# Kernel tuning notes

Measured on AMD Instinct MI355X. Metric: run time of the kernel, lower is better.

## Reference

```python
import jax, jax.numpy as jnp
import numpy as np

CHANS = [32, 32, 64, 64, 128, 128]
IN_CHANS = [1, 32, 32, 64, 64, 128]
BETA = 0.25  # VectorQuantizer_reset default; ResidualVQ's beta=0.4 is never forwarded
BN_EPS = 1e-5


def setup_inputs() -> dict:
    key = jax.random.key(0)
    ks = jax.random.split(key, 20)
    B, L, IDIM, H, NE = 64, 2000, 80, 256, 1024
    inp = {"speech": jax.random.normal(ks[0], (B, L, IDIM), jnp.float32)}
    for i, (ci, co) in enumerate(zip(IN_CHANS, CHANS)):
        inp[f"cw{i}"] = jax.random.normal(ks[1 + i], (co, ci, 3, 3), jnp.float32) * 0.05
        inp[f"g{i}"] = jnp.ones((co,), jnp.float32)
        inp[f"b{i}"] = jnp.zeros((co,), jnp.float32)
    inp["w_ih"] = jax.random.normal(ks[10], (3 * H, 256), jnp.float32) * 0.05
    inp["w_hh"] = jax.random.normal(ks[11], (3 * H, H), jnp.float32) * 0.05
    inp["bih"] = jnp.zeros((3 * H,), jnp.float32)
    inp["bhh"] = jnp.zeros((3 * H,), jnp.float32)
    for j, k in zip((1, 2, 3), (12, 13, 14)):
        inp[f"cb{j}"] = jax.random.uniform(ks[k], (NE, H), jnp.float32, -1.0 / NE, 1.0 / NE)
    return inp


def conv_bn_relu(x, w, g, b):
    # Conv2d(k=3, stride=2, pad=1, bias=False) + BatchNorm2d (training-mode batch stats) + ReLU
    y = jax.lax.conv_general_dilated(x, w, (2, 2), [(1, 1), (1, 1)],
                                     dimension_numbers=("NCHW", "OIHW", "NCHW"))
    mu = jnp.mean(y, axis=(0, 2, 3), keepdims=True)
    var = jnp.mean((y - mu) ** 2, axis=(0, 2, 3), keepdims=True)  # biased, as torch BN
    y = (y - mu) * jax.lax.rsqrt(var + BN_EPS) * g.reshape(1, -1, 1, 1) + b.reshape(1, -1, 1, 1)
    return jax.nn.relu(y)


def gru_last_hidden(x, w_ih, w_hh, bih, bhh):
    # x: (B, T, D). PyTorch GRU, 1 layer, h0 = 0; returns last hidden state (B, H).
    B = x.shape[0]
    H = w_hh.shape[1]
    xw = jnp.einsum("btd,gd->btg", x, w_ih) + bih  # (B, T, 3H), precompute input gates

    def step(h, xt):
        gh = h @ w_hh.T + bhh
        i_r, i_z, i_n = jnp.split(xt, 3, axis=-1)
        h_r, h_z, h_n = jnp.split(gh, 3, axis=-1)
        r = jax.nn.sigmoid(i_r + h_r)
        z = jax.nn.sigmoid(i_z + h_z)
        n = jnp.tanh(i_n + r * h_n)
        return (1.0 - z) * n + z * h, None

    h0 = jnp.zeros((B, H), x.dtype)
    hT, _ = jax.lax.scan(step, h0, jnp.swapaxes(xw, 0, 1))
    return hT


def vq(z, E):
    # z: (B, e_dim), E: (n_e, e_dim). Nearest-neighbor quantize + straight-through.
    d = jnp.sum(z * z, axis=1, keepdims=True) + jnp.sum(E * E, axis=1) - 2.0 * (z @ E.T)
    idx = jnp.argmin(d, axis=1)  # (B,)
    z_q = E[idx]
    loss = jnp.mean((jax.lax.stop_gradient(z_q) - z) ** 2) \
         + BETA * jnp.mean((z_q - jax.lax.stop_gradient(z)) ** 2)
    z_q_st = z + jax.lax.stop_gradient(z_q - z)
    return z_q_st, loss, idx


def reference(speech, cw0, g0, b0, cw1, g1, b1, cw2, g2, b2, cw3, g3, b3,
              cw4, g4, b4, cw5, g5, b5, w_ih, w_hh, bih, bhh, cb1, cb2, cb3):
    x = speech[:, None, :, :]  # (B, 1, L, idim)
    for w, g, b in ((cw0, g0, b0), (cw1, g1, b1), (cw2, g2, b2),
                    (cw3, g3, b3), (cw4, g4, b4), (cw5, g5, b5)):
        x = conv_bn_relu(x, w, g, b)
    B, C, T, F = x.shape
    hs = x.transpose(0, 2, 1, 3).reshape(B, T, C * F)  # (B, T', C*F)
    ref_embs = gru_last_hidden(hs, w_ih, w_hh, bih, bhh)  # (B, 256)

    residual = ref_embs
    zq1, l1, i1 = vq(residual, cb1)
    residual = residual - zq1
    zq2, l2, i2 = vq(residual, cb2)
    residual = residual - zq2
    zq3, l3, i3 = vq(residual, cb3)

    z_q_out = jnp.concatenate([zq1, zq2, zq3], axis=1)  # (B, 3*e_dim)
    vq_loss = l1 + l2 + l3
    codebooks = (zq1, zq2, zq3, zq1 + zq2 + zq3)
    return (z_q_out, vq_loss, i1[:, None], codebooks)
```

## Files before the change

### kernel.cpp

```cpp
#include <hip/hip_runtime.h>
#include <math.h>


__global__ void transpose_kernel(const float* __restrict__ in, float* __restrict__ out,
                                 int R, int C) {
  int n = R * C;
  for (int t = blockIdx.x * blockDim.x + threadIdx.x; t < n; t += gridDim.x * blockDim.x) {
    int i = t / C, j = t % C;
    out[j * R + i] = in[t];
  }
}

__global__ __launch_bounds__(256) void se_kernel(const float* __restrict__ ET,
                                                 float* __restrict__ sE) {
  int c = blockIdx.x * 256 + threadIdx.x;
  float s = 0.f;
  for (int k = 0; k < 256; ++k) {
    float v = ET[k * 1024 + c];
    s = fmaf(v, v, s);
  }
  sE[c] = s;
}

__global__ __launch_bounds__(256) void conv0_stats_kernel(
    const float* __restrict__ speech, const float* __restrict__ w0,
    float* __restrict__ part) {
  constexpr int TS = 81, TH = 49, TN = TH * TS;
  __shared__ float sp[TN];
  const int tid = threadIdx.x;
  const int bx = blockIdx.x;
  const int b = blockIdx.z;
  const int to0 = bx * 24;
  const int sr0 = 2 * to0 - 1;
  const float* sb = speech + (size_t)b * 2000 * 80;
  for (int i = tid; i < TN; i += 256) {
    int r = i / TS, c = i % TS;
    int gr = sr0 + r, gc = c - 1;
    sp[i] = (gr >= 0 && gr < 2000 && gc >= 0 && gc < 80) ? sb[gr * 80 + gc] : 0.f;
  }
  __syncthreads();

  const int fo = tid % 40;
  const int trr = tid / 40;
  const bool rowok = (trr < 6);
  const int r0 = rowok ? trr * 4 : 0;

  float xv4[4][9];
  {
    int sb0 = (2 * r0) * TS + 2 * fo;
    float p0 = sp[sb0], p1 = sp[sb0 + 1], p2 = sp[sb0 + 2];
#pragma unroll
    for (int k = 0; k < 4; ++k) {
      int mr = (2 * (r0 + k) + 1) * TS + 2 * fo;
      xv4[k][0] = p0; xv4[k][1] = p1; xv4[k][2] = p2;
      xv4[k][3] = sp[mr]; xv4[k][4] = sp[mr + 1]; xv4[k][5] = sp[mr + 2];
      xv4[k][6] = sp[mr + TS]; xv4[k][7] = sp[mr + TS + 1]; xv4[k][8] = sp[mr + TS + 2];
      p0 = xv4[k][6]; p1 = xv4[k][7]; p2 = xv4[k][8];
    }
  }
  bool val[4];
#pragma unroll
  for (int k = 0; k < 4; ++k) val[k] = rowok && (to0 + r0 + k < 1000);

  float s[32], q[32];
#pragma unroll
  for (int c = 0; c < 32; ++c) { s[c] = 0.f; q[c] = 0.f; }
#pragma unroll
  for (int c = 0; c < 32; ++c) {
    const float* wk = w0 + c * 9;
    float w0v = wk[0], w1v = wk[1], w2v = wk[2], w3v = wk[3], w4v = wk[4];
    float w5v = wk[5], w6v = wk[6], w7v = wk[7], w8v = wk[8];
#pragma unroll
    for (int k = 0; k < 4; ++k) {
      float a = xv4[k][0] * w0v;
      a = fmaf(xv4[k][1], w1v, a); a = fmaf(xv4[k][2], w2v, a);
      a = fmaf(xv4[k][3], w3v, a); a = fmaf(xv4[k][4], w4v, a);
      a = fmaf(xv4[k][5], w5v, a); a = fmaf(xv4[k][6], w6v, a);
      a = fmaf(xv4[k][7], w7v, a); a = fmaf(xv4[k][8], w8v, a);
      if (val[k]) { s[c] += a; q[c] = fmaf(a, a, q[c]); }
    }
  }
  const int wid = tid >> 6;
  const int lane = tid & 63;
  const int pidx = ((b * 42 + bx) << 2) | wid;
#pragma unroll
  for (int c = 0; c < 32; ++c) {
    float ss = s[c], qq = q[c];
#pragma unroll
    for (int m = 32; m >= 1; m >>= 1) {
      ss += __shfl_xor(ss, m, 64);
      qq += __shfl_xor(qq, m, 64);
    }
    if (lane == 0) {
      part[(size_t)c * 10752 + pidx] = ss;
      part[(size_t)(32 + c) * 10752 + pidx] = qq;
    }
  }
}

__global__ __launch_bounds__(256) void conv1_fused_kernel(
    const float* __restrict__ speech, const float* __restrict__ w0,
    const float* __restrict__ aff0, const float* __restrict__ w1,
    float* __restrict__ y) {
  constexpr int SPS = 81, SPH = 51, SPN = SPH * SPS;
  constexpr int LTS = 43, LTH = 25;
  __shared__ float sp[SPN];
  __shared__ float l0t[2][LTH * LTS];
  const int tid = threadIdx.x;
  const int bx = blockIdx.x;
  const int b = blockIdx.z;
  const int to0 = bx * 12;
  const int l0r0 = 2 * to0 - 1;
  const int sr0 = 4 * to0 - 3;
  const float* sb = speech + (size_t)b * 2000 * 80;
  for (int i = tid; i < SPN; i += 256) {
    int r = i / SPS, c = i % SPS;
    int gr = sr0 + r, gc = c - 1;
    sp[i] = (gr >= 0 && gr < 2000 && gc >= 0 && gc < 80) ? sb[gr * 80 + gc] : 0.f;
  }

  const int fc = tid % 42;
  const int fr0 = tid / 42;
  const bool filler = (tid < 210);
  const int wcol = fc - 1;
  const bool colok = (wcol >= 0) && (wcol < 40);
  const int spc = colok ? (2 * wcol) : 0;
  const int r0 = fr0 * 5;

  const int fo = tid % 20;
  const int tr = tid / 20;
  const int to = to0 + tr;
  const bool active = (tr < 12) && (to < 500);
  const int trc = (tr < 12) ? tr : 0;

  float acc[32];
#pragma unroll
  for (int c = 0; c < 32; ++c) acc[c] = 0.f;

  __syncthreads();

#define L0FILL(CIDX, BF)                                                      \
  if (filler) {                                                               \
    const float* wk = w0 + (CIDX) * 9;                                        \
    const float wv0 = wk[0], wv1 = wk[1], wv2 = wk[2], wv3 = wk[3];           \
    const float wv4 = wk[4], wv5 = wk[5], wv6 = wk[6], wv7 = wk[7];           \
    const float wv8 = wk[8];                                                  \
    const float sc = aff0[CIDX], sh = aff0[32 + (CIDX)];                      \
    int sb0 = (2 * r0) * SPS + spc;                                           \
    float t0 = sp[sb0], t1 = sp[sb0 + 1], t2 = sp[sb0 + 2];                   \
    _Pragma("unroll")                                                         \
    for (int k = 0; k < 5; ++k) {                                             \
      int r = r0 + k;                                                         \
      int mr = (2 * r + 1) * SPS + spc;                                       \
      float m0 = sp[mr], m1 = sp[mr + 1], m2 = sp[mr + 2];                    \
      float b0 = sp[mr + SPS], b1 = sp[mr + SPS + 1], b2 = sp[mr + SPS + 2];  \
      float a = t0 * wv0;                                                     \
      a = fmaf(t1, wv1, a); a = fmaf(t2, wv2, a);                             \
      a = fmaf(m0, wv3, a); a = fmaf(m1, wv4, a); a = fmaf(m2, wv5, a);       \
      a = fmaf(b0, wv6, a); a = fmaf(b1, wv7, a); a = fmaf(b2, wv8, a);       \
      int h0 = l0r0 + r;                                                      \
      bool ok = colok && h0 >= 0 && h0 < 1000;                                \
      float vv = ok ? fmaxf(fmaf(a, sc, sh), 0.f) : 0.f;                      \
      l0t[BF][r * LTS + fc] = vv;                                             \
      t0 = b0; t1 = b1; t2 = b2;                                              \
    }                                                                         \
  }

  L0FILL(0, 0)
  __syncthreads();

  for (int ci = 0; ci < 32; ++ci) {
    int cur = ci & 1;
    if (ci + 1 < 32) { L0FILL(ci + 1, cur ^ 1) }
    float xv[9];
    int base = 2 * trc * LTS + 2 * fo;
#pragma unroll
    for (int t = 0; t < 9; ++t) xv[t] = l0t[cur][base + (t / 3) * LTS + (t % 3)];
    const float* wp = w1 + ci * 9;
#pragma unroll
    for (int c = 0; c < 32; ++c) {
      const float* wc = wp + (size_t)c * 32 * 9;
#pragma unroll
      for (int t = 0; t < 9; ++t) acc[c] = fmaf(xv[t], wc[t], acc[c]);
    }
    __syncthreads();
  }
#undef L0FILL

  if (active) {
#pragma unroll
    for (int c = 0; c < 32; ++c)
      y[(((size_t)b * 32 + c) * 500 + to) * 20 + fo] = acc[c];
  }
}

template <int CI, int COG, int WO, int ROWS, int WI, int HI, int HO>
__global__ __launch_bounds__(256) void conv_kernel(
    const float* __restrict__ x, const float* __restrict__ w,
    const float* __restrict__ aff, float* __restrict__ y, int CO) {
  constexpr int TW = WI + 2;
  constexpr int TS = (TW & 1) ? TW : TW + 1;
  constexpr int TH = 2 * ROWS + 1;
  constexpr int TN = TH * TW;
  constexpr int F = (TN + 255) / 256;
  __shared__ float tile[2][TH * TS];

  const int tid = threadIdx.x;
  const int fo = tid % WO;
  const int tr = tid / WO;
  const int to0 = blockIdx.x * ROWS;
  const int to = to0 + tr;
  const int co0 = blockIdx.y * COG;
  const int b = blockIdx.z;
  const bool active = (tr < ROWS) && (to < HO);
  const int trc = (tr < ROWS) ? tr : 0;

  int fa[F], fof[F];
  bool fv[F], fw[F];
#pragma unroll
  for (int j = 0; j < F; ++j) {
    int i = tid + j * 256;
    int r = i / TW, c = i % TW;
    int gih = 2 * to0 - 1 + r;
    int giw = c - 1;
    bool inb = (i < TN);
    bool v = inb && gih >= 0 && gih < HI && giw >= 0 && giw < WI;
    fw[j] = inb;
    fv[j] = v;
    fof[j] = v ? (gih * WI + giw) : 0;
    fa[j] = inb ? (r * TS + c) : 0;
  }

  float acc[COG];
#pragma unroll
  for (int c = 0; c < COG; ++c) acc[c] = 0.f;

  const float* xb = x + (size_t)b * CI * HI * WI;

  {
    const float sc = aff[0], sh = aff[CI];
#pragma unroll
    for (int j = 0; j < F; ++j) {
      if (fw[j]) {
        float v = xb[fof[j]];
        v = fv[j] ? fmaxf(fmaf(v, sc, sh), 0.f) : 0.f;
        tile[0][fa[j]] = v;
      }
    }
  }
  __syncthreads();

  for (int ci = 0; ci < CI; ++ci) {
    int cur = ci & 1;
    if (ci + 1 < CI) {
      const float* xc = xb + (size_t)(ci + 1) * HI * WI;
      const float sc = aff[ci + 1], sh = aff[CI + ci + 1];
#pragma unroll
      for (int j = 0; j < F; ++j) {
        if (fw[j]) {
          float v = xc[fof[j]];
          v = fv[j] ? fmaxf(fmaf(v, sc, sh), 0.f) : 0.f;
          tile[cur ^ 1][fa[j]] = v;
        }
      }
    }
    float xv[9];
    int base = 2 * trc * TS + 2 * fo;
#pragma unroll
    for (int t = 0; t < 9; ++t) xv[t] = tile[cur][base + (t / 3) * TS + (t % 3)];
    const float* wp = w + ((size_t)co0 * CI + ci) * 9;
#pragma unroll
    for (int c = 0; c < COG; ++c) {
      const float* wc = wp + (size_t)c * CI * 9;
#pragma unroll
      for (int t = 0; t < 9; ++t) acc[c] = fmaf(xv[t], wc[t], acc[c]);
    }
    __syncthreads();
  }

  if (active) {
#pragma unroll
    for (int c = 0; c < COG; ++c)
      y[(((size_t)b * CO + co0 + c) * HO + to) * WO + fo] = acc[c];
  }
}

__global__ __launch_bounds__(256) void conv5_kernel(
    const float* __restrict__ x, const float* __restrict__ w5,
    const float* __restrict__ aff, float* __restrict__ part5) {
  constexpr int TS = 5, TH = 65, TN = TH * TS;
  __shared__ float tile[2][TN];
  const int tid = threadIdx.x;
  const int p = tid & 63;
  const int to = p >> 1, fo = p & 1;
  const int cog = tid >> 6;
  const int co0 = cog * 32;
  const int ci0 = blockIdx.y * 32;
  const int b = blockIdx.z;

  int fa[2], fof[2];
  bool fv[2], fw[2];
#pragma unroll
  for (int j = 0; j < 2; ++j) {
    int i = tid + j * 256;
    int r = i / TS, c = i % TS;
    int gih = r - 1, giw = c - 1;
    bool inb = (i < TN);
    bool v = inb && gih >= 0 && gih < 63 && giw >= 0 && giw < 3;
    fw[j] = inb; fv[j] = v;
    fof[j] = v ? (gih * 3 + giw) : 0;
    fa[j] = inb ? i : 0;
  }

  float acc[32];
#pragma unroll
  for (int c = 0; c < 32; ++c) acc[c] = 0.f;

  const float* xb = x + (size_t)b * 128 * 189;

  {
    const float sc = aff[ci0], sh = aff[128 + ci0];
    const float* xc = xb + (size_t)ci0 * 189;
#pragma unroll
    for (int j = 0; j < 2; ++j) {
      if (fw[j]) {
        float v = xc[fof[j]];
        v = fv[j] ? fmaxf(fmaf(v, sc, sh), 0.f) : 0.f;
        tile[0][fa[j]] = v;
      }
    }
  }
  __syncthreads();

  for (int cc = 0; cc < 32; ++cc) {
    int cur = cc & 1;
    int ci = ci0 + cc;
    if (cc + 1 < 32) {
      const float* xc = xb + (size_t)(ci + 1) * 189;
      const float sc = aff[ci + 1], sh = aff[128 + ci + 1];
#pragma unroll
      for (int j = 0; j < 2; ++j) {
        if (fw[j]) {
          float v = xc[fof[j]];
          v = fv[j] ? fmaxf(fmaf(v, sc, sh), 0.f) : 0.f;
          tile[cur ^ 1][fa[j]] = v;
        }
      }
    }
    float xv[9];
#pragma unroll
    for (int t = 0; t < 9; ++t)
      xv[t] = tile[cur][(2 * to + t / 3) * TS + 2 * fo + (t % 3)];
    const float* wp = w5 + ((size_t)co0 * 128 + ci) * 9;
#pragma unroll
    for (int c = 0; c < 32; ++c) {
      const float* wc = wp + (size_t)c * 128 * 9;
#pragma unroll
      for (int t = 0; t < 9; ++t) acc[c] = fmaf(xv[t], wc[t], acc[c]);
    }
    __syncthreads();
  }

#pragma unroll
  for (int c = 0; c < 32; ++c)
    part5[(((size_t)blockIdx.y * 64 + b) * 128 + co0 + c) * 64 + p] = acc[c];
}

__global__ __launch_bounds__(256) void reduce4_kernel(const float* __restrict__ p,
                                                      float* __restrict__ y) {
  int i = blockIdx.x * 256 + threadIdx.x;
  if (i < 524288)
    y[i] = p[i] + p[i + 524288] + p[i + 2 * 524288] + p[i + 3 * 524288];
}

__global__ __launch_bounds__(256) void stats_kernel(const float* __restrict__ x,
                                                    float* __restrict__ part,
                                                    int C, int HW) {
  int c = blockIdx.x, b = blockIdx.y, tid = threadIdx.x;
  const float* xb = x + ((size_t)b * C + c) * HW;
  float s = 0.f, q = 0.f;
  for (int i = tid; i < HW; i += 256) {
    float v = xb[i];
    s += v;
    q = fmaf(v, v, q);
  }
#pragma unroll
  for (int m = 32; m >= 1; m >>= 1) {
    s += __shfl_xor(s, m, 64);
    q += __shfl_xor(q, m, 64);
  }
  if ((tid & 63) == 0) {
    int w = tid >> 6;
    part[(size_t)c * 256 + b * 4 + w] = s;
    part[(size_t)(C + c) * 256 + b * 4 + w] = q;
  }
}

__global__ __launch_bounds__(256) void bn_finalize(
    const float* __restrict__ part, const float* __restrict__ g,
    const float* __restrict__ bb, float* __restrict__ aff, int CO, int P,
    double invN) {
  __shared__ double s1[256];
  __shared__ double s2[256];
  int c = blockIdx.x, tid = threadIdx.x;
  double a = 0, q = 0;
  for (int i = tid; i < P; i += 256) {
    a += (double)part[(size_t)c * P + i];
    q += (double)part[(size_t)(CO + c) * P + i];
  }
  s1[tid] = a;
  s2[tid] = q;
  __syncthreads();
  for (int s = 128; s > 0; s >>= 1) {
    if (tid < s) { s1[tid] += s1[tid + s]; s2[tid] += s2[tid + s]; }
    __syncthreads();
  }
  if (tid == 0) {
    double mean = s1[0] * invN;
    double var = s2[0] * invN - mean * mean;
    float scale = g[c] * (float)(1.0 / sqrt(var + 1e-5));
    aff[c] = scale;
    aff[CO + c] = bb[c] - (float)mean * scale;
  }
}

__global__ __launch_bounds__(256) void hs_kernel(const float* __restrict__ raw,
                                                 const float* __restrict__ aff5,
                                                 float* __restrict__ hs) {
  int i = blockIdx.x * 256 + threadIdx.x;
  if (i >= 524288) return;
  int b = i >> 13;
  int j = i & 8191;
  int t = j >> 8;
  int d = j & 255;
  int c = d >> 1;
  int f = d & 1;
  float sc = aff5[c], sh = aff5[128 + c];
  float v = raw[(((size_t)b * 128 + c) * 32 + t) * 2 + f];
  hs[i] = fmaxf(fmaf(v, sc, sh), 0.f);
}

__global__ __launch_bounds__(256) void xw_kernel(const float* __restrict__ hs,
                                                 const float* __restrict__ w_ihT,
                                                 const float* __restrict__ bih,
                                                 float* __restrict__ xw) {
  __shared__ float sh[8 * 256];
  int tid = threadIdx.x;
  int bt0 = blockIdx.x * 8;
  for (int i = tid; i < 8 * 256; i += 256) sh[i] = hs[(size_t)bt0 * 256 + i];
  __syncthreads();
  float acc[3][8];
#pragma unroll
  for (int g = 0; g < 3; ++g)
#pragma unroll
    for (int r = 0; r < 8; ++r) acc[g][r] = 0.f;
  for (int k = 0; k < 256; ++k) {
    float w0 = w_ihT[k * 768 + tid];
    float w1 = w_ihT[k * 768 + 256 + tid];
    float w2 = w_ihT[k * 768 + 512 + tid];
#pragma unroll
    for (int r = 0; r < 8; ++r) {
      float hv = sh[r * 256 + k];
      acc[0][r] = fmaf(hv, w0, acc[0][r]);
      acc[1][r] = fmaf(hv, w1, acc[1][r]);
      acc[2][r] = fmaf(hv, w2, acc[2][r]);
    }
  }
  float b0 = bih[tid], b1 = bih[256 + tid], b2 = bih[512 + tid];
  for (int r = 0; r < 8; ++r) {
    size_t base = (size_t)(bt0 + r) * 768;
    xw[base + tid] = acc[0][r] + b0;
    xw[base + 256 + tid] = acc[1][r] + b1;
    xw[base + 512 + tid] = acc[2][r] + b2;
  }
}

__global__ __launch_bounds__(768) void gru_kernel(const float* __restrict__ xw,
                                                  const float* __restrict__ w_hhT,
                                                  const float* __restrict__ bhh,
                                                  float* __restrict__ zout) {
  __shared__ __align__(16) float h[256];
  __shared__ float gh[768];
  int b = blockIdx.x, j = threadIdx.x;
  if (j < 256) h[j] = 0.f;
  __syncthreads();
  float bh = bhh[j];
  for (int t = 0; t < 32; ++t) {
    float acc = 0.f;
    const float4* h4 = (const float4*)h;
#pragma unroll 8
    for (int k4 = 0; k4 < 64; ++k4) {
      float4 hv = h4[k4];
      const float* wr = w_hhT + (4 * k4) * 768 + j;
      acc = fmaf(hv.x, wr[0], acc);
      acc = fmaf(hv.y, wr[768], acc);
      acc = fmaf(hv.z, wr[1536], acc);
      acc = fmaf(hv.w, wr[2304], acc);
    }
    gh[j] = acc + bh;
    __syncthreads();
    float hnew = 0.f;
    if (j < 256) {
      const float* xt = xw + ((size_t)b * 32 + t) * 768;
      float ir = xt[j], iz = xt[256 + j], inn = xt[512 + j];
      float r = 1.f / (1.f + expf(-(ir + gh[j])));
      float zz = 1.f / (1.f + expf(-(iz + gh[256 + j])));
      float n = tanhf(fmaf(r, gh[512 + j], inn));
      hnew = (1.f - zz) * n + zz * h[j];
    }
    __syncthreads();
    if (j < 256) h[j] = hnew;
    __syncthreads();
  }
  if (j < 256) zout[(size_t)b * 256 + j] = h[j];
}

template <int FIRST, int LAST>
__global__ __launch_bounds__(256) void vq_stage(
    const float* __restrict__ rin, const float* __restrict__ ET,
    const float* __restrict__ sE, const float* __restrict__ E,
    float* __restrict__ zq1, float* __restrict__ zq2, float* __restrict__ rout,
    float* __restrict__ msep, float* __restrict__ i1out,
    const float* __restrict__ z0, float* __restrict__ zqsum) {
  __shared__ float rz[256];
  __shared__ float rs[256];
  __shared__ int ri[256];
  __shared__ int bidx;
  int b = blockIdx.x, tid = threadIdx.x;
  rz[tid] = rin[(size_t)b * 256 + tid];
  __syncthreads();
  float a0 = 0.f, a1 = 0.f, a2 = 0.f, a3 = 0.f;
  for (int k = 0; k < 256; ++k) {
    float zk = rz[k];
    const float* row = ET + (size_t)k * 1024 + tid;
    a0 = fmaf(zk, row[0], a0);
    a1 = fmaf(zk, row[256], a1);
    a2 = fmaf(zk, row[512], a2);
    a3 = fmaf(zk, row[768], a3);
  }
  float s0 = sE[tid] - 2.f * a0;
  float s1 = sE[256 + tid] - 2.f * a1;
  float s2 = sE[512 + tid] - 2.f * a2;
  float s3 = sE[768 + tid] - 2.f * a3;
  float bs = s0;
  int bi = tid;
  if (s1 < bs) { bs = s1; bi = 256 + tid; }
  if (s2 < bs) { bs = s2; bi = 512 + tid; }
  if (s3 < bs) { bs = s3; bi = 768 + tid; }
  rs[tid] = bs;
  ri[tid] = bi;
  __syncthreads();
  for (int s = 128; s > 0; s >>= 1) {
    if (tid < s) {
      float os = rs[tid + s];
      int oi = ri[tid + s];
      if (os < rs[tid] || (os == rs[tid] && oi < ri[tid])) { rs[tid] = os; ri[tid] = oi; }
    }
    __syncthreads();
  }
  if (tid == 0) {
    bidx = ri[0];
    if (FIRST) i1out[b] = (float)ri[0];
  }
  __syncthreads();
  int idx = bidx;
  float zq = E[(size_t)idx * 256 + tid];
  float rv = rz[tid];
  float d = zq - rv;
  float rn = rv - zq;
  zq1[(size_t)b * 768 + tid] = zq;
  zq2[(size_t)b * 256 + tid] = zq;
  rout[(size_t)b * 256 + tid] = rn;
  if (LAST) zqsum[(size_t)b * 256 + tid] = z0[(size_t)b * 256 + tid] - rn;
  rs[tid] = d * d;
  __syncthreads();
  for (int s = 128; s > 0; s >>= 1) {
    if (tid < s) rs[tid] += rs[tid + s];
    __syncthreads();
  }
  if (tid == 0) msep[b] = rs[0];
}

__global__ void loss_kernel(const float* __restrict__ msep, float* __restrict__ out) {
  if (threadIdx.x == 0 && blockIdx.x == 0) {
    float s = 0.f;
    for (int i = 0; i < 192; ++i) s += msep[i];
    out[0] = 1.25f * s / 16384.0f;
  }
}

extern "C" void kernel_launch(void* const* d_in, const int* in_sizes, int n_in,
                              void* d_out, int out_size, void* d_ws, size_t ws_size,
                              hipStream_t stream) {
  const float* speech = (const float*)d_in[0];
  const float* cw[6];
  const float* gg[6];
  const float* bbp[6];
  for (int i = 0; i < 6; ++i) {
    cw[i] = (const float*)d_in[1 + 3 * i];
    gg[i] = (const float*)d_in[2 + 3 * i];
    bbp[i] = (const float*)d_in[3 + 3 * i];
  }
  const float* w_ih = (const float*)d_in[19];
  const float* w_hh = (const float*)d_in[20];
  const float* bih = (const float*)d_in[21];
  const float* bhh = (const float*)d_in[22];
  const float* cb[3] = {(const float*)d_in[23], (const float*)d_in[24], (const float*)d_in[25]};
  float* out = (float*)d_out;
  float* ws_f = (float*)d_ws;
  (void)in_sizes; (void)n_in; (void)out_size;

  size_t off = 0;
  float* act1 = ws_f + off; off += 20480000ull;
  float* act2 = ws_f + off; off += 10240000ull;
  float* act3 = ws_f + off; off += 2560000ull;
  float* part = ws_f + off; off += 700000ull;
  float* affs = ws_f + off; off += 1536ull;
  float* w_ihT = ws_f + off; off += 196608ull;
  float* w_hhT = ws_f + off; off += 196608ull;
  float* hs = ws_f + off; off += 524288ull;
  float* xw = ws_f + off; off += 1572864ull;
  float* zb = ws_f + off; off += 16384ull;
  float* rA = ws_f + off; off += 16384ull;
  float* rB = ws_f + off; off += 16384ull;
  float* ET0 = ws_f + off; off += 262144ull;
  float* ET1 = ws_f + off; off += 262144ull;
  float* ET2 = ws_f + off; off += 262144ull;
  float* sEp = ws_f + off; off += 3072ull;
  float* msep = ws_f + off; off += 192ull;

  if (ws_size < off * sizeof(float)) return;

  float* part5 = act1;
  float* act4 = act2;
  float* act5 = act3;

  const size_t OFF_LOSS = 49152;
  const size_t OFF_I1 = 49153;
  const size_t OFF_CB1 = 49217;
  const size_t OFF_CB2 = 65601;
  const size_t OFF_CB3 = 81985;
  const size_t OFF_CBSUM = 98369;

  transpose_kernel<<<256, 256, 0, stream>>>(w_ih, w_ihT, 768, 256);
  transpose_kernel<<<256, 256, 0, stream>>>(w_hh, w_hhT, 768, 256);
  transpose_kernel<<<256, 256, 0, stream>>>(cb[0], ET0, 1024, 256);
  transpose_kernel<<<256, 256, 0, stream>>>(cb[1], ET1, 1024, 256);
  transpose_kernel<<<256, 256, 0, stream>>>(cb[2], ET2, 1024, 256);
  se_kernel<<<4, 256, 0, stream>>>(ET0, sEp);
  se_kernel<<<4, 256, 0, stream>>>(ET1, sEp + 1024);
  se_kernel<<<4, 256, 0, stream>>>(ET2, sEp + 2048);

  conv0_stats_kernel<<<dim3(42, 1, 64), 256, 0, stream>>>(speech, cw[0], part);
  bn_finalize<<<32, 256, 0, stream>>>(part, gg[0], bbp[0], affs + 0, 32, 10752,
                                      1.0 / 2560000.0);
  conv1_fused_kernel<<<dim3(42, 1, 64), 256, 0, stream>>>(speech, cw[0], affs + 0,
                                                          cw[1], act1);
  stats_kernel<<<dim3(32, 64), 256, 0, stream>>>(act1, part, 32, 10000);
  bn_finalize<<<32, 256, 0, stream>>>(part, gg[1], bbp[1], affs + 256, 32, 256,
                                      1.0 / 640000.0);
  conv_kernel<32, 32, 10, 25, 20, 500, 250>
      <<<dim3(10, 2, 64), 256, 0, stream>>>(act1, cw[2], affs + 256, act2, 64);
  stats_kernel<<<dim3(64, 64), 256, 0, stream>>>(act2, part, 64, 2500);
  bn_finalize<<<64, 256, 0, stream>>>(part, gg[2], bbp[2], affs + 512, 64, 256,
                                      1.0 / 160000.0);
  conv_kernel<64, 16, 5, 42, 10, 250, 125>
      <<<dim3(3, 4, 64), 256, 0, stream>>>(act2, cw[3], affs + 512, act3, 64);
  stats_kernel<<<dim3(64, 64), 256, 0, stream>>>(act3, part, 64, 625);
  bn_finalize<<<64, 256, 0, stream>>>(part, gg[3], bbp[3], affs + 768, 64, 256,
                                      1.0 / 40000.0);
  conv_kernel<64, 16, 3, 63, 5, 125, 63>
      <<<dim3(1, 8, 64), 256, 0, stream>>>(act3, cw[4], affs + 768, act4, 128);
  stats_kernel<<<dim3(128, 64), 256, 0, stream>>>(act4, part, 128, 189);
  bn_finalize<<<128, 256, 0, stream>>>(part, gg[4], bbp[4], affs + 1024, 128, 256,
                                       1.0 / 12096.0);
  conv5_kernel<<<dim3(1, 4, 64), 256, 0, stream>>>(act4, cw[5], affs + 1024, part5);
  reduce4_kernel<<<2048, 256, 0, stream>>>(part5, act5);
  stats_kernel<<<dim3(128, 64), 256, 0, stream>>>(act5, part, 128, 64);
  bn_finalize<<<128, 256, 0, stream>>>(part, gg[5], bbp[5], affs + 1280, 128, 256,
                                       1.0 / 4096.0);

  hs_kernel<<<2048, 256, 0, stream>>>(act5, affs + 1280, hs);
  xw_kernel<<<256, 256, 0, stream>>>(hs, w_ihT, bih, xw);
  gru_kernel<<<64, 768, 0, stream>>>(xw, w_hhT, bhh, zb);

  vq_stage<1, 0><<<64, 256, 0, stream>>>(zb, ET0, sEp, cb[0], out + 0, out + OFF_CB1,
                                         rA, msep + 0, out + OFF_I1, nullptr, nullptr);
  vq_stage<0, 0><<<64, 256, 0, stream>>>(rA, ET1, sEp + 1024, cb[1], out + 256,
                                         out + OFF_CB2, rB, msep + 64, nullptr, nullptr,
                                         nullptr);
  vq_stage<0, 1><<<64, 256, 0, stream>>>(rB, ET2, sEp + 2048, cb[2], out + 512,
                                         out + OFF_CB3, rA, msep + 128, nullptr, zb,
                                         out + OFF_CBSUM);
  loss_kernel<<<1, 64, 0, stream>>>(msep, out + OFF_LOSS);
}
```

Before: 1.233 ms.

## Split conv shared tiles into even/odd column planes and fuse small kernels

```diff
diff --git a/kernel.cpp b/kernel.cpp
--- a/kernel.cpp
+++ b/kernel.cpp
@@ -2,41 +2,61 @@
 #include <math.h>
 
 
-__global__ void transpose_kernel(const float* __restrict__ in, float* __restrict__ out,
-                                 int R, int C) {
-  int n = R * C;
-  for (int t = blockIdx.x * blockDim.x + threadIdx.x; t < n; t += gridDim.x * blockDim.x) {
-    int i = t / C, j = t % C;
-    out[j * R + i] = in[t];
-  }
-}
-
-__global__ __launch_bounds__(256) void se_kernel(const float* __restrict__ ET,
-                                                 float* __restrict__ sE) {
-  int c = blockIdx.x * 256 + threadIdx.x;
-  float s = 0.f;
-  for (int k = 0; k < 256; ++k) {
-    float v = ET[k * 1024 + c];
-    s = fmaf(v, v, s);
-  }
-  sE[c] = s;
+__global__ __launch_bounds__(256) void prep_kernel(
+    const float* __restrict__ w_ih, const float* __restrict__ w_hh,
+    const float* __restrict__ cb0, const float* __restrict__ cb1,
+    const float* __restrict__ cb2, float* __restrict__ w_ihT,
+    float* __restrict__ w_hhT, float* __restrict__ ET, float* __restrict__ sE) {
+  int tid = threadIdx.x;
+  int y = blockIdx.y;
+  if (y < 5) {
+    const float* in;
+    float* outp;
+    int R, C;
+    if (y == 0) { in = w_ih; outp = w_ihT; R = 768; C = 256; }
+    else if (y == 1) { in = w_hh; outp = w_hhT; R = 768; C = 256; }
+    else {
+      in = (y == 2 ? cb0 : (y == 3 ? cb1 : cb2));
+      outp = ET + (size_t)(y - 2) * 262144;
+      R = 1024; C = 256;
+    }
+    int n = R * C;
+    for (int t = blockIdx.x * 256 + tid; t < n; t += 64 * 256) {
+      int i = t / C, j = t % C;
+      outp[(size_t)j * R + i] = in[t];
+    }
+  } else {
+    int wid = tid >> 6, lane = tid & 63;
+    for (int c = blockIdx.x * 4 + wid; c < 3072; c += 64 * 4) {
+      const float* E = (c < 1024 ? cb0 : (c < 2048 ? cb1 : cb2));
+      int cc = c & 1023;
+      float4 v4 = ((const float4*)(E + (size_t)cc * 256))[lane];
+      float ssum = v4.x * v4.x + v4.y * v4.y + v4.z * v4.z + v4.w * v4.w;
+#pragma unroll
+      for (int m = 32; m >= 1; m >>= 1) ssum += __shfl_xor(ssum, m, 64);
+      if (lane == 0) sE[c] = ssum;
+    }
+  }
 }
 
 __global__ __launch_bounds__(256) void conv0_stats_kernel(
     const float* __restrict__ speech, const float* __restrict__ w0,
     float* __restrict__ part) {
-  constexpr int TS = 81, TH = 49, TN = TH * TS;
-  __shared__ float sp[TN];
+  constexpr int SPR = 41, SPH = 49;
+  __shared__ float spE[SPH * SPR];
+  __shared__ float spO[SPH * SPR];
   const int tid = threadIdx.x;
   const int bx = blockIdx.x;
   const int b = blockIdx.z;
   const int to0 = bx * 24;
   const int sr0 = 2 * to0 - 1;
-  const float* sb = speech + (size_t)b * 2000 * 80;
-  for (int i = tid; i < TN; i += 256) {
-    int r = i / TS, c = i % TS;
+  const float* sb = speech + (size_t)b * 160000;
+  for (int i = tid; i < SPH * 81; i += 256) {
+    int r = i / 81, c = i % 81;
     int gr = sr0 + r, gc = c - 1;
-    sp[i] = (gr >= 0 && gr < 2000 && gc >= 0 && gc < 80) ? sb[gr * 80 + gc] : 0.f;
+    float v = (gr >= 0 && gr < 2000 && gc >= 0 && gc < 80) ? sb[gr * 80 + gc] : 0.f;
+    float* pl = (c & 1) ? spO : spE;
+    pl[r * SPR + (c >> 1)] = v;
   }
   __syncthreads();
 
@@ -47,14 +67,15 @@
 
   float xv4[4][9];
   {
-    int sb0 = (2 * r0) * TS + 2 * fo;
-    float p0 = sp[sb0], p1 = sp[sb0 + 1], p2 = sp[sb0 + 2];
+    int e0 = (2 * r0) * SPR + fo;
+    float p0 = spE[e0], p1 = spO[e0], p2 = spE[e0 + 1];
 #pragma unroll
     for (int k = 0; k < 4; ++k) {
-      int mr = (2 * (r0 + k) + 1) * TS + 2 * fo;
+      int mr = (2 * (r0 + k) + 1) * SPR + fo;
+      int br = mr + SPR;
       xv4[k][0] = p0; xv4[k][1] = p1; xv4[k][2] = p2;
-      xv4[k][3] = sp[mr]; xv4[k][4] = sp[mr + 1]; xv4[k][5] = sp[mr + 2];
-      xv4[k][6] = sp[mr + TS]; xv4[k][7] = sp[mr + TS + 1]; xv4[k][8] = sp[mr + TS + 2];
+      xv4[k][3] = spE[mr]; xv4[k][4] = spO[mr]; xv4[k][5] = spE[mr + 1];
+      xv4[k][6] = spE[br]; xv4[k][7] = spO[br]; xv4[k][8] = spE[br + 1];
       p0 = xv4[k][6]; p1 = xv4[k][7]; p2 = xv4[k][8];
     }
   }
@@ -102,21 +123,24 @@
     const float* __restrict__ speech, const float* __restrict__ w0,
     const float* __restrict__ aff0, const float* __restrict__ w1,
     float* __restrict__ y) {
-  constexpr int SPS = 81, SPH = 51, SPN = SPH * SPS;
-  constexpr int LTS = 43, LTH = 25;
-  __shared__ float sp[SPN];
-  __shared__ float l0t[2][LTH * LTS];
+  constexpr int SPR = 41, SPH = 51;
+  constexpr int LPS = 21, LTH = 25, LPL = LTH * LPS;
+  __shared__ float spE[SPH * SPR];
+  __shared__ float spO[SPH * SPR];
+  __shared__ float l0t[2][2 * LPL];
   const int tid = threadIdx.x;
   const int bx = blockIdx.x;
   const int b = blockIdx.z;
   const int to0 = bx * 12;
   const int l0r0 = 2 * to0 - 1;
   const int sr0 = 4 * to0 - 3;
-  const float* sb = speech + (size_t)b * 2000 * 80;
-  for (int i = tid; i < SPN; i += 256) {
-    int r = i / SPS, c = i % SPS;
+  const float* sb = speech + (size_t)b * 160000;
+  for (int i = tid; i < SPH * 81; i += 256) {
+    int r = i / 81, c = i % 81;
     int gr = sr0 + r, gc = c - 1;
-    sp[i] = (gr >= 0 && gr < 2000 && gc >= 0 && gc < 80) ? sb[gr * 80 + gc] : 0.f;
+    float v = (gr >= 0 && gr < 2000 && gc >= 0 && gc < 80) ? sb[gr * 80 + gc] : 0.f;
+    float* pl = (c & 1) ? spO : spE;
+    pl[r * SPR + (c >> 1)] = v;
   }
 
   const int fc = tid % 42;
@@ -124,8 +148,10 @@
   const bool filler = (tid < 210);
   const int wcol = fc - 1;
   const bool colok = (wcol >= 0) && (wcol < 40);
-  const int spc = colok ? (2 * wcol) : 0;
+  const int wc = colok ? wcol : 0;
   const int r0 = fr0 * 5;
+  const int lplane = (fc & 1) * LPL;
+  const int lidx = fc >> 1;
 
   const int fo = tid % 20;
   const int tr = tid / 20;
@@ -146,14 +172,15 @@
     const float wv4 = wk[4], wv5 = wk[5], wv6 = wk[6], wv7 = wk[7];           \
     const float wv8 = wk[8];                                                  \
     const float sc = aff0[CIDX], sh = aff0[32 + (CIDX)];                      \
-    int sb0 = (2 * r0) * SPS + spc;                                           \
-    float t0 = sp[sb0], t1 = sp[sb0 + 1], t2 = sp[sb0 + 2];                   \
+    int e0 = (2 * r0) * SPR + wc;                                             \
+    float t0 = spE[e0], t1 = spO[e0], t2 = spE[e0 + 1];                       \
     _Pragma("unroll")                                                         \
     for (int k = 0; k < 5; ++k) {                                             \
       int r = r0 + k;                                                         \
-      int mr = (2 * r + 1) * SPS + spc;                                       \
-      float m0 = sp[mr], m1 = sp[mr + 1], m2 = sp[mr + 2];                    \
-      float b0 = sp[mr + SPS], b1 = sp[mr + SPS + 1], b2 = sp[mr + SPS + 2];  \
+      int mr = (2 * r + 1) * SPR + wc;                                        \
+      int br = mr + SPR;                                                      \
+      float m0 = spE[mr], m1 = spO[mr], m2 = spE[mr + 1];                     \
+      float b0 = spE[br], b1 = spO[br], b2 = spE[br + 1];                     \
       float a = t0 * wv0;                                                     \
       a = fmaf(t1, wv1, a); a = fmaf(t2, wv2, a);                             \
       a = fmaf(m0, wv3, a); a = fmaf(m1, wv4, a); a = fmaf(m2, wv5, a);       \
@@ -161,7 +188,7 @@
       int h0 = l0r0 + r;                                                      \
       bool ok = colok && h0 >= 0 && h0 < 1000;                                \
       float vv = ok ? fmaxf(fmaf(a, sc, sh), 0.f) : 0.f;                      \
-      l0t[BF][r * LTS + fc] = vv;                                             \
+      l0t[BF][lplane + r * LPS + lidx] = vv;                                  \
       t0 = b0; t1 = b1; t2 = b2;                                              \
     }                                                                         \
   }
@@ -173,15 +200,18 @@
     int cur = ci & 1;
     if (ci + 1 < 32) { L0FILL(ci + 1, cur ^ 1) }
     float xv[9];
-    int base = 2 * trc * LTS + 2 * fo;
-#pragma unroll
-    for (int t = 0; t < 9; ++t) xv[t] = l0t[cur][base + (t / 3) * LTS + (t % 3)];
+    const int rb = 2 * trc;
+#pragma unroll
+    for (int t = 0; t < 9; ++t) {
+      int dr = t / 3, m = t % 3;
+      xv[t] = l0t[cur][(m == 1 ? LPL : 0) + (rb + dr) * LPS + fo + (m == 2 ? 1 : 0)];
+    }
     const float* wp = w1 + ci * 9;
 #pragma unroll
     for (int c = 0; c < 32; ++c) {
-      const float* wc = wp + (size_t)c * 32 * 9;
-#pragma unroll
-      for (int t = 0; t < 9; ++t) acc[c] = fmaf(xv[t], wc[t], acc[c]);
+      const float* wcp = wp + (size_t)c * 32 * 9;
+#pragma unroll
+      for (int t = 0; t < 9; ++t) acc[c] = fmaf(xv[t], wcp[t], acc[c]);
     }
     __syncthreads();
   }
@@ -199,11 +229,13 @@
     const float* __restrict__ x, const float* __restrict__ w,
     const float* __restrict__ aff, float* __restrict__ y, int CO) {
   constexpr int TW = WI + 2;
-  constexpr int TS = (TW & 1) ? TW : TW + 1;
+  constexpr int PE = (TW + 1) / 2;
+  constexpr int PS = PE | 1;
   constexpr int TH = 2 * ROWS + 1;
+  constexpr int PL = TH * PS;
   constexpr int TN = TH * TW;
   constexpr int F = (TN + 255) / 256;
-  __shared__ float tile[2][TH * TS];
+  __shared__ float tile[2][2 * PL];
 
   const int tid = threadIdx.x;
   const int fo = tid % WO;
@@ -228,7 +260,7 @@
     fw[j] = inb;
     fv[j] = v;
     fof[j] = v ? (gih * WI + giw) : 0;
-    fa[j] = inb ? (r * TS + c) : 0;
+    fa[j] = inb ? ((c & 1) * PL + r * PS + (c >> 1)) : 0;
   }
 
   float acc[COG];
@@ -265,9 +297,12 @@
       }
     }
     float xv[9];
-    int base = 2 * trc * TS + 2 * fo;
-#pragma unroll
-    for (int t = 0; t < 9; ++t) xv[t] = tile[cur][base + (t / 3) * TS + (t % 3)];
+    const int rb = 2 * trc;
+#pragma unroll
+    for (int t = 0; t < 9; ++t) {
+      int dr = t / 3, m = t % 3;
+      xv[t] = tile[cur][(m == 1 ? PL : 0) + (rb + dr) * PS + fo + (m == 2 ? 1 : 0)];
+    }
     const float* wp = w + ((size_t)co0 * CI + ci) * 9;
 #pragma unroll
     for (int c = 0; c < COG; ++c) {
@@ -288,8 +323,8 @@
 __global__ __launch_bounds__(256) void conv5_kernel(
     const float* __restrict__ x, const float* __restrict__ w5,
     const float* __restrict__ aff, float* __restrict__ part5) {
-  constexpr int TS = 5, TH = 65, TN = TH * TS;
-  __shared__ float tile[2][TN];
+  constexpr int TW = 5, PS = 3, TH = 65, PL = TH * PS, TN = TH * TW;
+  __shared__ float tile[2][2 * PL];
   const int tid = threadIdx.x;
   const int p = tid & 63;
   const int to = p >> 1, fo = p & 1;
@@ -303,13 +338,14 @@
 #pragma unroll
   for (int j = 0; j < 2; ++j) {
     int i = tid + j * 256;
-    int r = i / TS, c = i % TS;
+    int r = i / TW, c = i % TW;
     int gih = r - 1, giw = c - 1;
     bool inb = (i < TN);
     bool v = inb && gih >= 0 && gih < 63 && giw >= 0 && giw < 3;
-    fw[j] = inb; fv[j] = v;
+    fw[j] = inb;
+    fv[j] = v;
     fof[j] = v ? (gih * 3 + giw) : 0;
-    fa[j] = inb ? i : 0;
+    fa[j] = inb ? ((c & 1) * PL + r * PS + (c >> 1)) : 0;
   }
 
   float acc[32];
@@ -349,8 +385,10 @@
     }
     float xv[9];
 #pragma unroll
-    for (int t = 0; t < 9; ++t)
-      xv[t] = tile[cur][(2 * to + t / 3) * TS + 2 * fo + (t % 3)];
+    for (int t = 0; t < 9; ++t) {
+      int dr = t / 3, m = t % 3;
+      xv[t] = tile[cur][(m == 1 ? PL : 0) + (2 * to + dr) * PS + fo + (m == 2 ? 1 : 0)];
+    }
     const float* wp = w5 + ((size_t)co0 * 128 + ci) * 9;
 #pragma unroll
     for (int c = 0; c < 32; ++c) {
@@ -424,30 +462,21 @@
   }
 }
 
-__global__ __launch_bounds__(256) void hs_kernel(const float* __restrict__ raw,
+__global__ __launch_bounds__(256) void xw_kernel(const float* __restrict__ act5,
                                                  const float* __restrict__ aff5,
-                                                 float* __restrict__ hs) {
-  int i = blockIdx.x * 256 + threadIdx.x;
-  if (i >= 524288) return;
-  int b = i >> 13;
-  int j = i & 8191;
-  int t = j >> 8;
-  int d = j & 255;
-  int c = d >> 1;
-  int f = d & 1;
-  float sc = aff5[c], sh = aff5[128 + c];
-  float v = raw[(((size_t)b * 128 + c) * 32 + t) * 2 + f];
-  hs[i] = fmaxf(fmaf(v, sc, sh), 0.f);
-}
-
-__global__ __launch_bounds__(256) void xw_kernel(const float* __restrict__ hs,
                                                  const float* __restrict__ w_ihT,
                                                  const float* __restrict__ bih,
                                                  float* __restrict__ xw) {
   __shared__ float sh[8 * 256];
   int tid = threadIdx.x;
   int bt0 = blockIdx.x * 8;
-  for (int i = tid; i < 8 * 256; i += 256) sh[i] = hs[(size_t)bt0 * 256 + i];
+  int b = bt0 >> 5;
+  for (int i = tid; i < 2048; i += 256) {
+    int r = i >> 8, d = i & 255, c = d >> 1, f = d & 1;
+    int t = (bt0 + r) & 31;
+    float v = act5[(((size_t)b * 128 + c) * 32 + t) * 2 + f];
+    sh[i] = fmaxf(fmaf(v, aff5[c], aff5[128 + c]), 0.f);
+  }
   __syncthreads();
   float acc[3][8];
 #pragma unroll
@@ -499,86 +528,89 @@
     }
     gh[j] = acc + bh;
     __syncthreads();
-    float hnew = 0.f;
     if (j < 256) {
       const float* xt = xw + ((size_t)b * 32 + t) * 768;
       float ir = xt[j], iz = xt[256 + j], inn = xt[512 + j];
       float r = 1.f / (1.f + expf(-(ir + gh[j])));
       float zz = 1.f / (1.f + expf(-(iz + gh[256 + j])));
       float n = tanhf(fmaf(r, gh[512 + j], inn));
-      hnew = (1.f - zz) * n + zz * h[j];
-    }
-    __syncthreads();
-    if (j < 256) h[j] = hnew;
+      h[j] = (1.f - zz) * n + zz * h[j];
+    }
     __syncthreads();
   }
   if (j < 256) zout[(size_t)b * 256 + j] = h[j];
 }
 
-template <int FIRST, int LAST>
-__global__ __launch_bounds__(256) void vq_stage(
-    const float* __restrict__ rin, const float* __restrict__ ET,
-    const float* __restrict__ sE, const float* __restrict__ E,
-    float* __restrict__ zq1, float* __restrict__ zq2, float* __restrict__ rout,
-    float* __restrict__ msep, float* __restrict__ i1out,
-    const float* __restrict__ z0, float* __restrict__ zqsum) {
+__global__ __launch_bounds__(256) void vq_all_kernel(
+    const float* __restrict__ zb, const float* __restrict__ ET,
+    const float* __restrict__ sE, const float* __restrict__ cb0,
+    const float* __restrict__ cb1, const float* __restrict__ cb2,
+    float* __restrict__ out, float* __restrict__ msep) {
+  const size_t OFF_I1 = 49153;
+  const size_t OFF_CB = 49217;
+  const size_t OFF_CBSUM = 98369;
   __shared__ float rz[256];
   __shared__ float rs[256];
   __shared__ int ri[256];
-  __shared__ int bidx;
   int b = blockIdx.x, tid = threadIdx.x;
-  rz[tid] = rin[(size_t)b * 256 + tid];
-  __syncthreads();
-  float a0 = 0.f, a1 = 0.f, a2 = 0.f, a3 = 0.f;
-  for (int k = 0; k < 256; ++k) {
-    float zk = rz[k];
-    const float* row = ET + (size_t)k * 1024 + tid;
-    a0 = fmaf(zk, row[0], a0);
-    a1 = fmaf(zk, row[256], a1);
-    a2 = fmaf(zk, row[512], a2);
-    a3 = fmaf(zk, row[768], a3);
-  }
-  float s0 = sE[tid] - 2.f * a0;
-  float s1 = sE[256 + tid] - 2.f * a1;
-  float s2 = sE[512 + tid] - 2.f * a2;
-  float s3 = sE[768 + tid] - 2.f * a3;
-  float bs = s0;
-  int bi = tid;
-  if (s1 < bs) { bs = s1; bi = 256 + tid; }
-  if (s2 < bs) { bs = s2; bi = 512 + tid; }
-  if (s3 < bs) { bs = s3; bi = 768 + tid; }
-  rs[tid] = bs;
-  ri[tid] = bi;
-  __syncthreads();
-  for (int s = 128; s > 0; s >>= 1) {
-    if (tid < s) {
-      float os = rs[tid + s];
-      int oi = ri[tid + s];
-      if (os < rs[tid] || (os == rs[tid] && oi < ri[tid])) { rs[tid] = os; ri[tid] = oi; }
-    }
-    __syncthreads();
-  }
-  if (tid == 0) {
-    bidx = ri[0];
-    if (FIRST) i1out[b] = (float)ri[0];
-  }
-  __syncthreads();
-  int idx = bidx;
-  float zq = E[(size_t)idx * 256 + tid];
-  float rv = rz[tid];
-  float d = zq - rv;
-  float rn = rv - zq;
-  zq1[(size_t)b * 768 + tid] = zq;
-  zq2[(size_t)b * 256 + tid] = zq;
-  rout[(size_t)b * 256 + tid] = rn;
-  if (LAST) zqsum[(size_t)b * 256 + tid] = z0[(size_t)b * 256 + tid] - rn;
-  rs[tid] = d * d;
-  __syncthreads();
-  for (int s = 128; s > 0; s >>= 1) {
-    if (tid < s) rs[tid] += rs[tid + s];
-    __syncthreads();
-  }
-  if (tid == 0) msep[b] = rs[0];
+  float z0 = zb[(size_t)b * 256 + tid];
+  rz[tid] = z0;
+  float zqs = 0.f;
+  for (int s = 0; s < 3; ++s) {
+    __syncthreads();
+    const float* ETs = ET + (size_t)s * 262144;
+    const float* sEs = sE + s * 1024;
+    const float* E = (s == 0 ? cb0 : (s == 1 ? cb1 : cb2));
+    float a0 = 0.f, a1 = 0.f, a2 = 0.f, a3 = 0.f;
+    for (int k = 0; k < 256; ++k) {
+      float zk = rz[k];
+      const float* row = ETs + (size_t)k * 1024 + tid;
+      a0 = fmaf(zk, row[0], a0);
+      a1 = fmaf(zk, row[256], a1);
+      a2 = fmaf(zk, row[512], a2);
+      a3 = fmaf(zk, row[768], a3);
+    }
+    float s0 = sEs[tid] - 2.f * a0;
+    float s1 = sEs[256 + tid] - 2.f * a1;
+    float s2 = sEs[512 + tid] - 2.f * a2;
+    float s3 = sEs[768 + tid] - 2.f * a3;
+    float bs = s0;
+    int bi = tid;
+    if (s1 < bs) { bs = s1; bi = 256 + tid; }
+    if (s2 < bs) { bs = s2; bi = 512 + tid; }
+    if (s3 < bs) { bs = s3; bi = 768 + tid; }
+    rs[tid] = bs;
+    ri[tid] = bi;
+    __syncthreads();
+    for (int st = 128; st > 0; st >>= 1) {
+      if (tid < st) {
+        float os = rs[tid + st];
+        int oi = ri[tid + st];
+        if (os < rs[tid] || (os == rs[tid] && oi < ri[tid])) {
+          rs[tid] = os;
+          ri[tid] = oi;
+        }
+      }
+      __syncthreads();
+    }
+    int idx = ri[0];
+    if (s == 0 && tid == 0) out[OFF_I1 + b] = (float)idx;
+    float zq = E[(size_t)idx * 256 + tid];
+    float rv = rz[tid];
+    float d = zq - rv;
+    out[(size_t)b * 768 + s * 256 + tid] = zq;
+    out[OFF_CB + (size_t)s * 16384 + (size_t)b * 256 + tid] = zq;
+    zqs += zq;
+    rz[tid] = rv - zq;
+    rs[tid] = d * d;
+    __syncthreads();
+    for (int st = 128; st > 0; st >>= 1) {
+      if (tid < st) rs[tid] += rs[tid + st];
+      __syncthreads();
+    }
+    if (tid == 0) msep[s * 64 + b] = rs[0];
+  }
+  out[OFF_CBSUM + (size_t)b * 256 + tid] = zqs;
 }
 
 __global__ void loss_kernel(const float* __restrict__ msep, float* __restrict__ out) {
@@ -618,14 +650,9 @@
   float* affs = ws_f + off; off += 1536ull;
   float* w_ihT = ws_f + off; off += 196608ull;
   float* w_hhT = ws_f + off; off += 196608ull;
-  float* hs = ws_f + off; off += 524288ull;
   float* xw = ws_f + off; off += 1572864ull;
   float* zb = ws_f + off; off += 16384ull;
-  float* rA = ws_f + off; off += 16384ull;
-  float* rB = ws_f + off; off += 16384ull;
-  float* ET0 = ws_f + off; off += 262144ull;
-  float* ET1 = ws_f + off; off += 262144ull;
-  float* ET2 = ws_f + off; off += 262144ull;
+  float* ET = ws_f + off; off += 786432ull;
   float* sEp = ws_f + off; off += 3072ull;
   float* msep = ws_f + off; off += 192ull;
 
@@ -636,20 +663,9 @@
   float* act5 = act3;
 
   const size_t OFF_LOSS = 49152;
-  const size_t OFF_I1 = 49153;
-  const size_t OFF_CB1 = 49217;
-  const size_t OFF_CB2 = 65601;
-  const size_t OFF_CB3 = 81985;
-  const size_t OFF_CBSUM = 98369;
-
-  transpose_kernel<<<256, 256, 0, stream>>>(w_ih, w_ihT, 768, 256);
-  transpose_kernel<<<256, 256, 0, stream>>>(w_hh, w_hhT, 768, 256);
-  transpose_kernel<<<256, 256, 0, stream>>>(cb[0], ET0, 1024, 256);
-  transpose_kernel<<<256, 256, 0, stream>>>(cb[1], ET1, 1024, 256);
-  transpose_kernel<<<256, 256, 0, stream>>>(cb[2], ET2, 1024, 256);
-  se_kernel<<<4, 256, 0, stream>>>(ET0, sEp);
-  se_kernel<<<4, 256, 0, stream>>>(ET1, sEp + 1024);
-  se_kernel<<<4, 256, 0, stream>>>(ET2, sEp + 2048);
+
+  prep_kernel<<<dim3(64, 6), 256, 0, stream>>>(w_ih, w_hh, cb[0], cb[1], cb[2],
+                                               w_ihT, w_hhT, ET, sEp);
 
   conv0_stats_kernel<<<dim3(42, 1, 64), 256, 0, stream>>>(speech, cw[0], part);
   bn_finalize<<<32, 256, 0, stream>>>(part, gg[0], bbp[0], affs + 0, 32, 10752,
@@ -680,17 +696,9 @@
   bn_finalize<<<128, 256, 0, stream>>>(part, gg[5], bbp[5], affs + 1280, 128, 256,
                                        1.0 / 4096.0);
 
-  hs_kernel<<<2048, 256, 0, stream>>>(act5, affs + 1280, hs);
-  xw_kernel<<<256, 256, 0, stream>>>(hs, w_ihT, bih, xw);
+  xw_kernel<<<256, 256, 0, stream>>>(act5, affs + 1280, w_ihT, bih, xw);
   gru_kernel<<<64, 768, 0, stream>>>(xw, w_hhT, bhh, zb);
 
-  vq_stage<1, 0><<<64, 256, 0, stream>>>(zb, ET0, sEp, cb[0], out + 0, out + OFF_CB1,
-                                         rA, msep + 0, out + OFF_I1, nullptr, nullptr);
-  vq_stage<0, 0><<<64, 256, 0, stream>>>(rA, ET1, sEp + 1024, cb[1], out + 256,
-                                         out + OFF_CB2, rB, msep + 64, nullptr, nullptr,
-                                         nullptr);
-  vq_stage<0, 1><<<64, 256, 0, stream>>>(rB, ET2, sEp + 2048, cb[2], out + 512,
-                                         out + OFF_CB3, rA, msep + 128, nullptr, zb,
-                                         out + OFF_CBSUM);
+  vq_all_kernel<<<64, 256, 0, stream>>>(zb, ET, sEp, cb[0], cb[1], cb[2], out, msep);
   loss_kernel<<<1, 64, 0, stream>>>(msep, out + OFF_LOSS);
 }
```

After: 1.182 ms. 1.04x faster.
